# Kernel optimization log

Measured on AMD Instinct MI355X. Metric: run time of the kernel, lower is better.

The kernel has to match this reference:

```python
import jax, jax.numpy as jnp
import numpy as np

E, K = 8, 2
B, S, H = 8, 2048, 512
R0, R1, O = 256, 256, 512
T = B * S


def _make_routing(key):
    # Mixtral-style: top-k softmax weights [T, K] and one-hot mask [E, K, T]
    k1, k2 = jax.random.split(key)
    sel = jax.random.randint(k1, (T, K), 0, E)                      # selected expert per (token, slot)
    rw = jax.nn.softmax(jax.random.normal(k2, (T, K)), axis=-1)
    mask = jax.nn.one_hot(sel, E, dtype=jnp.bool_)                  # [T, K, E]
    mask = jnp.transpose(mask, (2, 1, 0))                           # [E, K, T]
    return mask, rw


def setup_inputs() -> dict:
    key = jax.random.key(0)
    ks = jax.random.split(key, 10)
    x = jax.random.normal(ks[0], (B, S, H), dtype=jnp.float32)
    m1, rw1 = _make_routing(ks[1])
    m2, rw2 = _make_routing(ks[2])
    m3, rw3 = _make_routing(ks[3])
    s = 0.02
    W1 = jax.random.normal(ks[4], (E, R0, H), dtype=jnp.float32) * s
    b1 = jnp.zeros((E, R0), dtype=jnp.float32)
    W2 = jax.random.normal(ks[5], (E, R1, R0), dtype=jnp.float32) * s
    b2 = jnp.zeros((E, R1), dtype=jnp.float32)
    W3 = jax.random.normal(ks[6], (E, O, R1), dtype=jnp.float32) * s
    b3 = jnp.zeros((E, O), dtype=jnp.float32)
    return {"x": x,
            "expert_mask1": m1, "expert_mask2": m2, "expert_mask3": m3,
            "routing_weights1": rw1, "routing_weights2": rw2, "routing_weights3": rw3,
            "W1": W1, "b1": b1, "W2": W2, "b2": b2, "W3": W3, "b3": b3}


def _moe_stage(h, mask, rw, W, b, act):
    # combine[e, t] = routing weight of token t for expert e (0 if not routed)
    cmb = jnp.einsum('ekt,tk->et', mask.astype(h.dtype), rw)
    acc0 = jnp.zeros((h.shape[0], W.shape[1]), dtype=h.dtype)

    def body(acc, ew):
        Wi, bi, ci = ew            # Wi: [out, in], bi: [out], ci: [T]
        out = h @ Wi.T + bi
        if act:
            out = jax.nn.relu(out)
        return acc + ci[:, None] * out, None

    acc, _ = jax.lax.scan(body, acc0, (W, b, cmb))
    return acc


def reference(x, expert_mask1, expert_mask2, expert_mask3,
              routing_weights1, routing_weights2, routing_weights3,
              W1, b1, W2, b2, W3, b3):
    bsz, seq, dim = x.shape
    h = x.reshape(-1, dim)                                          # [T, H]
    h = _moe_stage(h, expert_mask1, routing_weights1, W1, b1, act=False)   # [T, R0]
    h = _moe_stage(h, expert_mask2, routing_weights2, W2, b2, act=False)   # [T, R1]
    h = _moe_stage(h, expert_mask3, routing_weights3, W3, b3, act=True)    # relu on expert output, then combine
    out = jax.nn.relu(h.reshape(bsz, seq, -1))
    return out
```

## Files before the change

### kernel.cpp

```cpp
#include <hip/hip_runtime.h>

#define T_TOKENS 16384
#define CAP 12288
#define RB 96
#define CNT_STRIDE 16

typedef unsigned short u16;
typedef unsigned int u32;
typedef __attribute__((ext_vector_type(8))) short short8;
typedef __attribute__((ext_vector_type(4))) float float4v;

typedef __attribute__((address_space(1))) u32 gas_u32;
typedef __attribute__((address_space(3))) u32 las_u32;

__device__ __forceinline__ u16 f2b(float f) {
  unsigned u = __float_as_uint(f);
  u = (u + 0x7fffu + ((u >> 16) & 1u)) >> 16;
  return (u16)u;
}
__device__ __forceinline__ float b2f(u16 h) {
  return __uint_as_float(((unsigned)h) << 16);
}
__device__ __forceinline__ void gload16(const u16* g, u16* l) {
  __builtin_amdgcn_global_load_lds((gas_u32*)g, (las_u32*)l, 16, 0, 0);
}

__global__ void prep_kernel(const float* __restrict__ W1, const float* __restrict__ W2,
                            const float* __restrict__ W3,
                            const int* __restrict__ m1, const int* __restrict__ m2,
                            const int* __restrict__ m3, const float* __restrict__ rw1,
                            const float* __restrict__ rw2, const float* __restrict__ rw3,
                            u16* __restrict__ Wb1, u16* __restrict__ Wb2, u16* __restrict__ Wb3,
                            int* __restrict__ cnt, int* __restrict__ idxbuf,
                            float* __restrict__ wgtbuf) {
  __shared__ int lcnt[24];
  __shared__ int lbase[24];
  const int tid = threadIdx.x;

  if (blockIdx.x >= 64) {
    const int n1 = 8 * 256 * 512, n2 = 8 * 256 * 256;
    int base = (blockIdx.x - 64) * 2048 + tid * 8;
    const float* src;
    u16* dst;
    int off = base;
    if (base < n1) { src = W1; dst = Wb1; }
    else if (base < n1 + n2) { src = W2; dst = Wb2; off = base - n1; }
    else { src = W3; dst = Wb3; off = base - n1 - n2; }
    float4 a0 = *(const float4*)(src + off);
    float4 a1 = *(const float4*)(src + off + 4);
    short8 v;
    v[0] = (short)f2b(a0.x); v[1] = (short)f2b(a0.y);
    v[2] = (short)f2b(a0.z); v[3] = (short)f2b(a0.w);
    v[4] = (short)f2b(a1.x); v[5] = (short)f2b(a1.y);
    v[6] = (short)f2b(a1.z); v[7] = (short)f2b(a1.w);
    *(short8*)(dst + off) = v;
    return;
  }

  const int t = blockIdx.x * 256 + tid;
  if (tid < 24) lcnt[tid] = 0;
  __syncthreads();

  const int* masks[3] = {m1, m2, m3};
  const float* rws[3] = {rw1, rw2, rw3};
  int expert[3][2], lpos[3][2];
#pragma unroll
  for (int s = 0; s < 3; ++s)
#pragma unroll
    for (int k = 0; k < 2; ++k) {
      int e = 0;
#pragma unroll
      for (int j = 0; j < 8; ++j)
        if (masks[s][(j * 2 + k) * T_TOKENS + t] != 0) e = j;
      expert[s][k] = e;
      lpos[s][k] = atomicAdd(&lcnt[s * 8 + e], 1);
    }
  __syncthreads();
  if (tid < 24) lbase[tid] = atomicAdd(&cnt[tid * CNT_STRIDE], lcnt[tid]);
  __syncthreads();
#pragma unroll
  for (int s = 0; s < 3; ++s)
#pragma unroll
    for (int k = 0; k < 2; ++k) {
      int e = expert[s][k];
      int p = lbase[s * 8 + e] + lpos[s][k];
      if (p < CAP) {
        idxbuf[(s * 8 + e) * CAP + p] = t * 2 + k;
        wgtbuf[(s * 8 + e) * CAP + p] = rws[s][t * 2 + k];
      }
    }
}

template <int KDIM, int NDIM_TOTAL, int SRC, int RELU>
__global__ __launch_bounds__(256) void moe_gemm(
    const void* __restrict__ Asrc, const u16* __restrict__ Wb, const float* __restrict__ bias,
    const int* __restrict__ cnt, const int* __restrict__ idxbuf, const float* __restrict__ wgtbuf,
    u16* __restrict__ outTmp) {
  __shared__ __align__(16) u16 As[64 * 64];
  __shared__ __align__(16) u16 Bs[256 * 64];
  __shared__ int rowTok[64];
  __shared__ float rowW[64];

  const int e = blockIdx.y;
  const int n_e = cnt[e * CNT_STRIDE];
  const int row0 = blockIdx.x * 64;
  if (row0 >= n_e) return;
  const int nbase = blockIdx.z * 256;
  const int tid = threadIdx.x;

  if (tid < 64) {
    int g = row0 + tid;
    if (g < n_e) {
      rowTok[tid] = idxbuf[e * CAP + g];
      rowW[tid] = wgtbuf[e * CAP + g];
    } else {
      rowTok[tid] = 0;
      rowW[tid] = 0.f;
    }
  }
  __syncthreads();

  const int wave = tid >> 6, lane = tid & 63;
  const int lrow = lane & 15, lquad = lane >> 4;
  const int srow = lane >> 3;
  const int gswl = (lane & 7) ^ srow;

  const u16* Wbe = Wb + ((size_t)e * NDIM_TOTAL + nbase) * KDIM;
  const u16* bP = Wbe + (size_t)(wave * 64 + srow) * KDIM + gswl * 8;
  u16* bD = Bs + (wave * 8) * 512;

  const int arow = tid >> 3;
  const int gsrc = tid & 7;

  float4v acc[4][4];
#pragma unroll
  for (int i = 0; i < 4; ++i)
#pragma unroll
    for (int j = 0; j < 4; ++j) acc[i][j] = (float4v)0.f;

  for (int kb = 0; kb < KDIM; kb += 64) {
#pragma unroll
    for (int i = 0; i < 8; ++i)
      gload16(bP + (size_t)i * 8 * KDIM + kb, bD + i * 512);
#pragma unroll
    for (int it = 0; it < 2; ++it) {
      int r = arow + it * 32;
      int tok = rowTok[r];
      int slot = gsrc ^ (r & 7);
      short8 v;
      if (SRC == 0) {
        const float* xp = (const float*)Asrc + (size_t)(tok >> 1) * KDIM + kb + gsrc * 8;
        float4 a0 = *(const float4*)xp;
        float4 a1 = *(const float4*)(xp + 4);
        v[0] = (short)f2b(a0.x); v[1] = (short)f2b(a0.y);
        v[2] = (short)f2b(a0.z); v[3] = (short)f2b(a0.w);
        v[4] = (short)f2b(a1.x); v[5] = (short)f2b(a1.y);
        v[6] = (short)f2b(a1.z); v[7] = (short)f2b(a1.w);
      } else {
        const u16* p0 = (const u16*)Asrc + ((size_t)(tok >> 1) * 2) * KDIM + kb + gsrc * 8;
        short8 v0 = *(const short8*)p0;
        short8 v1 = *(const short8*)(p0 + KDIM);
#pragma unroll
        for (int j = 0; j < 8; ++j)
          v[j] = (short)f2b(b2f((u16)v0[j]) + b2f((u16)v1[j]));
      }
      *(short8*)&As[r * 64 + slot * 8] = v;
    }
    __syncthreads();
#pragma unroll
    for (int ks = 0; ks < 64; ks += 32) {
      const int gq = ((ks >> 3) + lquad) ^ (lrow & 7);
      short8 af[4], bfr[4];
#pragma unroll
      for (int mt = 0; mt < 4; ++mt)
        af[mt] = *(const short8*)&As[(mt * 16 + lrow) * 64 + gq * 8];
#pragma unroll
      for (int nt = 0; nt < 4; ++nt)
        bfr[nt] = *(const short8*)&Bs[(wave * 64 + nt * 16 + lrow) * 64 + gq * 8];
#pragma unroll
      for (int mt = 0; mt < 4; ++mt)
#pragma unroll
        for (int nt = 0; nt < 4; ++nt)
          acc[mt][nt] = __builtin_amdgcn_mfma_f32_16x16x32_bf16(af[mt], bfr[nt], acc[mt][nt], 0, 0, 0);
    }
    __syncthreads();
  }

  float bv[4];
#pragma unroll
  for (int nt = 0; nt < 4; ++nt)
    bv[nt] = bias[e * NDIM_TOTAL + nbase + wave * 64 + nt * 16 + lrow];
#pragma unroll
  for (int mt = 0; mt < 4; ++mt) {
#pragma unroll
    for (int i = 0; i < 4; ++i) {
      int m = mt * 16 + lquad * 4 + i;
      if (row0 + m < n_e) {
        float w = rowW[m];
        size_t drow = (size_t)rowTok[m] * NDIM_TOTAL + nbase;
#pragma unroll
        for (int nt = 0; nt < 4; ++nt) {
          float v = acc[mt][nt][i] + bv[nt];
          if (RELU) v = fmaxf(v, 0.f);
          v *= w;
          outTmp[drow + wave * 64 + nt * 16 + lrow] = f2b(v);
        }
      }
    }
  }
}

__global__ void finalize_kernel(const u16* __restrict__ tmp3, float* __restrict__ out) {
  int f = (blockIdx.x * 256 + threadIdx.x) * 8;
  int t = f >> 9;
  int o = f & 511;
  const u16* p = tmp3 + (size_t)t * 1024 + o;
  short8 v0 = *(const short8*)p;
  short8 v1 = *(const short8*)(p + 512);
  float4 r0, r1;
  r0.x = fmaxf(b2f((u16)v0[0]) + b2f((u16)v1[0]), 0.f);
  r0.y = fmaxf(b2f((u16)v0[1]) + b2f((u16)v1[1]), 0.f);
  r0.z = fmaxf(b2f((u16)v0[2]) + b2f((u16)v1[2]), 0.f);
  r0.w = fmaxf(b2f((u16)v0[3]) + b2f((u16)v1[3]), 0.f);
  r1.x = fmaxf(b2f((u16)v0[4]) + b2f((u16)v1[4]), 0.f);
  r1.y = fmaxf(b2f((u16)v0[5]) + b2f((u16)v1[5]), 0.f);
  r1.z = fmaxf(b2f((u16)v0[6]) + b2f((u16)v1[6]), 0.f);
  r1.w = fmaxf(b2f((u16)v0[7]) + b2f((u16)v1[7]), 0.f);
  *(float4*)(out + f) = r0;
  *(float4*)(out + f + 4) = r1;
}

extern "C" void kernel_launch(void* const* d_in, const int* in_sizes, int n_in,
                              void* d_out, int out_size, void* d_ws, size_t ws_size,
                              hipStream_t stream) {
  const float* x  = (const float*)d_in[0];
  const int* m1   = (const int*)d_in[1];
  const int* m2   = (const int*)d_in[2];
  const int* m3   = (const int*)d_in[3];
  const float* rw1 = (const float*)d_in[4];
  const float* rw2 = (const float*)d_in[5];
  const float* rw3 = (const float*)d_in[6];
  const float* W1 = (const float*)d_in[7];
  const float* b1 = (const float*)d_in[8];
  const float* W2 = (const float*)d_in[9];
  const float* b2 = (const float*)d_in[10];
  const float* W3 = (const float*)d_in[11];
  const float* b3 = (const float*)d_in[12];
  float* out = (float*)d_out;

  char* ws = (char*)d_ws;
  size_t off = 0;
  int* cnt = (int*)(ws + off); off += 24 * CNT_STRIDE * 4;
  u16* Wb1 = (u16*)(ws + off); off += (size_t)8 * 256 * 512 * 2;
  u16* Wb2 = (u16*)(ws + off); off += (size_t)8 * 256 * 256 * 2;
  u16* Wb3 = (u16*)(ws + off); off += (size_t)8 * 512 * 256 * 2;
  u16* tmp1 = (u16*)(ws + off); off += (size_t)T_TOKENS * 2 * 256 * 2;
  u16* tmp2 = (u16*)(ws + off); off += (size_t)T_TOKENS * 2 * 256 * 2;
  u16* tmp3 = (u16*)(ws + off); off += (size_t)T_TOKENS * 2 * 512 * 2;
  int* idxb = (int*)(ws + off); off += (size_t)3 * 8 * CAP * 4;
  float* wgtb = (float*)(ws + off); off += (size_t)3 * 8 * CAP * 4;

  hipMemsetAsync(cnt, 0, 24 * CNT_STRIDE * 4, stream);
  prep_kernel<<<1344, 256, 0, stream>>>(W1, W2, W3, m1, m2, m3, rw1, rw2, rw3,
                                        Wb1, Wb2, Wb3, cnt, idxb, wgtb);

  moe_gemm<512, 256, 0, 0><<<dim3(RB, 8, 1), 256, 0, stream>>>(
      x, Wb1, b1, cnt + 0, idxb + 0, wgtb + 0, tmp1);
  moe_gemm<256, 256, 1, 0><<<dim3(RB, 8, 1), 256, 0, stream>>>(
      tmp1, Wb2, b2, cnt + 8 * CNT_STRIDE, idxb + 8 * CAP, wgtb + 8 * CAP, tmp2);
  moe_gemm<256, 512, 1, 1><<<dim3(RB, 8, 2), 256, 0, stream>>>(
      tmp2, Wb3, b3, cnt + 16 * CNT_STRIDE, idxb + 16 * CAP, wgtb + 16 * CAP, tmp3);

  finalize_kernel<<<4096, 256, 0, stream>>>(tmp3, out);
}
```

Measured before the change: 184.2 us.

## Drop LDS staging in MoE GEMM and load MFMA fragments directly from global

The MoE GEMM no longer stages A and B tiles through shared memory. Each lane now loads its MFMA operand fragments straight from global memory using per-row token pointers, which removes the barriers and the LDS traffic. The input x is converted to bf16 once in the prep kernel, so stage 1 reads bf16 instead of converting fp32 inside the GEMM. The cost is that the four waves no longer share staged tiles, so there are redundant global/L2 reads of A and B, uncoalesced gathers, and extra bandwidth for the x conversion pass.

```diff
diff --git a/kernel.cpp b/kernel.cpp
--- a/kernel.cpp
+++ b/kernel.cpp
@@ -10,9 +10,6 @@
 typedef __attribute__((ext_vector_type(8))) short short8;
 typedef __attribute__((ext_vector_type(4))) float float4v;
 
-typedef __attribute__((address_space(1))) u32 gas_u32;
-typedef __attribute__((address_space(3))) u32 las_u32;
-
 __device__ __forceinline__ u16 f2b(float f) {
   unsigned u = __float_as_uint(f);
   u = (u + 0x7fffu + ((u >> 16) & 1u)) >> 16;
@@ -21,16 +18,14 @@
 __device__ __forceinline__ float b2f(u16 h) {
   return __uint_as_float(((unsigned)h) << 16);
 }
-__device__ __forceinline__ void gload16(const u16* g, u16* l) {
-  __builtin_amdgcn_global_load_lds((gas_u32*)g, (las_u32*)l, 16, 0, 0);
-}
 
 __global__ void prep_kernel(const float* __restrict__ W1, const float* __restrict__ W2,
-                            const float* __restrict__ W3,
+                            const float* __restrict__ W3, const float* __restrict__ x,
                             const int* __restrict__ m1, const int* __restrict__ m2,
                             const int* __restrict__ m3, const float* __restrict__ rw1,
                             const float* __restrict__ rw2, const float* __restrict__ rw3,
                             u16* __restrict__ Wb1, u16* __restrict__ Wb2, u16* __restrict__ Wb3,
+                            u16* __restrict__ xb,
                             int* __restrict__ cnt, int* __restrict__ idxbuf,
                             float* __restrict__ wgtbuf) {
   __shared__ int lcnt[24];
@@ -38,14 +33,15 @@
   const int tid = threadIdx.x;
 
   if (blockIdx.x >= 64) {
-    const int n1 = 8 * 256 * 512, n2 = 8 * 256 * 256;
+    const int n1 = 8 * 256 * 512, n2 = 8 * 256 * 256, n3 = 8 * 512 * 256;
     int base = (blockIdx.x - 64) * 2048 + tid * 8;
     const float* src;
     u16* dst;
     int off = base;
     if (base < n1) { src = W1; dst = Wb1; }
     else if (base < n1 + n2) { src = W2; dst = Wb2; off = base - n1; }
-    else { src = W3; dst = Wb3; off = base - n1 - n2; }
+    else if (base < n1 + n2 + n3) { src = W3; dst = Wb3; off = base - n1 - n2; }
+    else { src = x; dst = xb; off = base - n1 - n2 - n3; }
     float4 a0 = *(const float4*)(src + off);
     float4 a1 = *(const float4*)(src + off + 4);
     short8 v;
@@ -92,45 +88,36 @@
 }
 
 template <int KDIM, int NDIM_TOTAL, int SRC, int RELU>
-__global__ __launch_bounds__(256) void moe_gemm(
-    const void* __restrict__ Asrc, const u16* __restrict__ Wb, const float* __restrict__ bias,
+__global__ void moe_gemm(
+    const u16* __restrict__ Asrc, const u16* __restrict__ Wb, const float* __restrict__ bias,
     const int* __restrict__ cnt, const int* __restrict__ idxbuf, const float* __restrict__ wgtbuf,
     u16* __restrict__ outTmp) {
-  __shared__ __align__(16) u16 As[64 * 64];
-  __shared__ __align__(16) u16 Bs[256 * 64];
-  __shared__ int rowTok[64];
-  __shared__ float rowW[64];
-
   const int e = blockIdx.y;
   const int n_e = cnt[e * CNT_STRIDE];
   const int row0 = blockIdx.x * 64;
   if (row0 >= n_e) return;
   const int nbase = blockIdx.z * 256;
   const int tid = threadIdx.x;
-
-  if (tid < 64) {
-    int g = row0 + tid;
-    if (g < n_e) {
-      rowTok[tid] = idxbuf[e * CAP + g];
-      rowW[tid] = wgtbuf[e * CAP + g];
+  const int wc = tid >> 6, lane = tid & 63;
+  const int lrow = lane & 15, lquad = lane >> 4;
+
+  const u16* aB0[4];
+  const u16* aB1[4];
+#pragma unroll
+  for (int mt = 0; mt < 4; ++mt) {
+    int g = row0 + mt * 16 + lrow;
+    int tok = (g < n_e) ? idxbuf[e * CAP + g] : 0;
+    if constexpr (SRC == 0) {
+      aB0[mt] = Asrc + (size_t)(tok >> 1) * KDIM + lquad * 8;
     } else {
-      rowTok[tid] = 0;
-      rowW[tid] = 0.f;
-    }
-  }
-  __syncthreads();
-
-  const int wave = tid >> 6, lane = tid & 63;
-  const int lrow = lane & 15, lquad = lane >> 4;
-  const int srow = lane >> 3;
-  const int gswl = (lane & 7) ^ srow;
-
-  const u16* Wbe = Wb + ((size_t)e * NDIM_TOTAL + nbase) * KDIM;
-  const u16* bP = Wbe + (size_t)(wave * 64 + srow) * KDIM + gswl * 8;
-  u16* bD = Bs + (wave * 8) * 512;
-
-  const int arow = tid >> 3;
-  const int gsrc = tid & 7;
+      aB0[mt] = Asrc + ((size_t)(tok >> 1) * 2) * KDIM + lquad * 8;
+      aB1[mt] = aB0[mt] + KDIM;
+    }
+  }
+  const u16* bB[4];
+#pragma unroll
+  for (int nt = 0; nt < 4; ++nt)
+    bB[nt] = Wb + ((size_t)e * NDIM_TOTAL + nbase + wc * 64 + nt * 16 + lrow) * KDIM + lquad * 8;
 
   float4v acc[4][4];
 #pragma unroll
@@ -138,72 +125,50 @@
 #pragma unroll
     for (int j = 0; j < 4; ++j) acc[i][j] = (float4v)0.f;
 
-  for (int kb = 0; kb < KDIM; kb += 64) {
-#pragma unroll
-    for (int i = 0; i < 8; ++i)
-      gload16(bP + (size_t)i * 8 * KDIM + kb, bD + i * 512);
-#pragma unroll
-    for (int it = 0; it < 2; ++it) {
-      int r = arow + it * 32;
-      int tok = rowTok[r];
-      int slot = gsrc ^ (r & 7);
-      short8 v;
-      if (SRC == 0) {
-        const float* xp = (const float*)Asrc + (size_t)(tok >> 1) * KDIM + kb + gsrc * 8;
-        float4 a0 = *(const float4*)xp;
-        float4 a1 = *(const float4*)(xp + 4);
-        v[0] = (short)f2b(a0.x); v[1] = (short)f2b(a0.y);
-        v[2] = (short)f2b(a0.z); v[3] = (short)f2b(a0.w);
-        v[4] = (short)f2b(a1.x); v[5] = (short)f2b(a1.y);
-        v[6] = (short)f2b(a1.z); v[7] = (short)f2b(a1.w);
+#pragma unroll 2
+  for (int kb = 0; kb < KDIM; kb += 32) {
+    short8 af[4], bf[4];
+#pragma unroll
+    for (int mt = 0; mt < 4; ++mt) {
+      if constexpr (SRC == 0) {
+        af[mt] = *(const short8*)(aB0[mt] + kb);
       } else {
-        const u16* p0 = (const u16*)Asrc + ((size_t)(tok >> 1) * 2) * KDIM + kb + gsrc * 8;
-        short8 v0 = *(const short8*)p0;
-        short8 v1 = *(const short8*)(p0 + KDIM);
+        short8 u = *(const short8*)(aB0[mt] + kb);
+        short8 w = *(const short8*)(aB1[mt] + kb);
 #pragma unroll
         for (int j = 0; j < 8; ++j)
-          v[j] = (short)f2b(b2f((u16)v0[j]) + b2f((u16)v1[j]));
+          af[mt][j] = (short)f2b(b2f((u16)u[j]) + b2f((u16)w[j]));
       }
-      *(short8*)&As[r * 64 + slot * 8] = v;
-    }
-    __syncthreads();
-#pragma unroll
-    for (int ks = 0; ks < 64; ks += 32) {
-      const int gq = ((ks >> 3) + lquad) ^ (lrow & 7);
-      short8 af[4], bfr[4];
-#pragma unroll
-      for (int mt = 0; mt < 4; ++mt)
-        af[mt] = *(const short8*)&As[(mt * 16 + lrow) * 64 + gq * 8];
+    }
+#pragma unroll
+    for (int nt = 0; nt < 4; ++nt)
+      bf[nt] = *(const short8*)(bB[nt] + kb);
+#pragma unroll
+    for (int mt = 0; mt < 4; ++mt)
 #pragma unroll
       for (int nt = 0; nt < 4; ++nt)
-        bfr[nt] = *(const short8*)&Bs[(wave * 64 + nt * 16 + lrow) * 64 + gq * 8];
-#pragma unroll
-      for (int mt = 0; mt < 4; ++mt)
-#pragma unroll
-        for (int nt = 0; nt < 4; ++nt)
-          acc[mt][nt] = __builtin_amdgcn_mfma_f32_16x16x32_bf16(af[mt], bfr[nt], acc[mt][nt], 0, 0, 0);
-    }
-    __syncthreads();
+        acc[mt][nt] = __builtin_amdgcn_mfma_f32_16x16x32_bf16(af[mt], bf[nt], acc[mt][nt], 0, 0, 0);
   }
 
   float bv[4];
 #pragma unroll
   for (int nt = 0; nt < 4; ++nt)
-    bv[nt] = bias[e * NDIM_TOTAL + nbase + wave * 64 + nt * 16 + lrow];
+    bv[nt] = bias[e * NDIM_TOTAL + nbase + wc * 64 + nt * 16 + lrow];
 #pragma unroll
   for (int mt = 0; mt < 4; ++mt) {
 #pragma unroll
     for (int i = 0; i < 4; ++i) {
       int m = mt * 16 + lquad * 4 + i;
-      if (row0 + m < n_e) {
-        float w = rowW[m];
-        size_t drow = (size_t)rowTok[m] * NDIM_TOTAL + nbase;
+      int g = row0 + m;
+      if (g < n_e) {
+        float w = wgtbuf[e * CAP + g];
+        size_t drow = (size_t)idxbuf[e * CAP + g] * NDIM_TOTAL + nbase;
 #pragma unroll
         for (int nt = 0; nt < 4; ++nt) {
           float v = acc[mt][nt][i] + bv[nt];
           if (RELU) v = fmaxf(v, 0.f);
           v *= w;
-          outTmp[drow + wave * 64 + nt * 16 + lrow] = f2b(v);
+          outTmp[drow + wc * 64 + nt * 16 + lrow] = f2b(v);
         }
       }
     }
@@ -254,6 +219,7 @@
   u16* Wb1 = (u16*)(ws + off); off += (size_t)8 * 256 * 512 * 2;
   u16* Wb2 = (u16*)(ws + off); off += (size_t)8 * 256 * 256 * 2;
   u16* Wb3 = (u16*)(ws + off); off += (size_t)8 * 512 * 256 * 2;
+  u16* xb  = (u16*)(ws + off); off += (size_t)T_TOKENS * 512 * 2;
   u16* tmp1 = (u16*)(ws + off); off += (size_t)T_TOKENS * 2 * 256 * 2;
   u16* tmp2 = (u16*)(ws + off); off += (size_t)T_TOKENS * 2 * 256 * 2;
   u16* tmp3 = (u16*)(ws + off); off += (size_t)T_TOKENS * 2 * 512 * 2;
@@ -261,11 +227,11 @@
   float* wgtb = (float*)(ws + off); off += (size_t)3 * 8 * CAP * 4;
 
   hipMemsetAsync(cnt, 0, 24 * CNT_STRIDE * 4, stream);
-  prep_kernel<<<1344, 256, 0, stream>>>(W1, W2, W3, m1, m2, m3, rw1, rw2, rw3,
-                                        Wb1, Wb2, Wb3, cnt, idxb, wgtb);
+  prep_kernel<<<5440, 256, 0, stream>>>(W1, W2, W3, x, m1, m2, m3, rw1, rw2, rw3,
+                                        Wb1, Wb2, Wb3, xb, cnt, idxb, wgtb);
 
   moe_gemm<512, 256, 0, 0><<<dim3(RB, 8, 1), 256, 0, stream>>>(
-      x, Wb1, b1, cnt + 0, idxb + 0, wgtb + 0, tmp1);
+      xb, Wb1, b1, cnt + 0, idxb + 0, wgtb + 0, tmp1);
   moe_gemm<256, 256, 1, 0><<<dim3(RB, 8, 1), 256, 0, stream>>>(
       tmp1, Wb2, b2, cnt + 8 * CNT_STRIDE, idxb + 8 * CAP, wgtb + 8 * CAP, tmp2);
   moe_gemm<256, 512, 1, 1><<<dim3(RB, 8, 2), 256, 0, stream>>>(
```

Result: slower. 332.9 us (+80.8%).

## Split K dimension across blocks in first two MoE GEMM stages

Applied to the files above, without the earlier changes.

Stages 1 and 2 now split the reduction dimension into two halves, each run by its own block along grid z. Each half writes a separate partial output slot per token, so the intermediate buffers grow to four slots per token. The next stage sums all four slots while loading its A tile, and only the first half adds the bias. This doubles the block count for the underfilled early stages, at the cost of extra bf16 partial writes, more reads in the following stage, and an extra bf16 rounding of each partial.

```diff
diff --git a/kernel.cpp b/kernel.cpp
--- a/kernel.cpp
+++ b/kernel.cpp
@@ -91,7 +91,7 @@
     }
 }
 
-template <int KDIM, int NDIM_TOTAL, int SRC, int RELU>
+template <int KDIM, int NDIM_TOTAL, int SRC, int RELU, int KSPLIT, int SLOTS_IN>
 __global__ __launch_bounds__(256) void moe_gemm(
     const void* __restrict__ Asrc, const u16* __restrict__ Wb, const float* __restrict__ bias,
     const int* __restrict__ cnt, const int* __restrict__ idxbuf, const float* __restrict__ wgtbuf,
@@ -105,7 +105,10 @@
   const int n_e = cnt[e * CNT_STRIDE];
   const int row0 = blockIdx.x * 64;
   if (row0 >= n_e) return;
-  const int nbase = blockIdx.z * 256;
+  const int khalf = (KSPLIT > 1) ? blockIdx.z : 0;
+  const int nbase = (KSPLIT > 1) ? 0 : blockIdx.z * 256;
+  const int kbase = khalf * (KDIM / KSPLIT);
+  const int KLEN = KDIM / KSPLIT;
   const int tid = threadIdx.x;
 
   if (tid < 64) {
@@ -126,7 +129,7 @@
   const int gswl = (lane & 7) ^ srow;
 
   const u16* Wbe = Wb + ((size_t)e * NDIM_TOTAL + nbase) * KDIM;
-  const u16* bP = Wbe + (size_t)(wave * 64 + srow) * KDIM + gswl * 8;
+  const u16* bP = Wbe + (size_t)(wave * 64 + srow) * KDIM + kbase + gswl * 8;
   u16* bD = Bs + (wave * 8) * 512;
 
   const int arow = tid >> 3;
@@ -138,7 +141,7 @@
 #pragma unroll
     for (int j = 0; j < 4; ++j) acc[i][j] = (float4v)0.f;
 
-  for (int kb = 0; kb < KDIM; kb += 64) {
+  for (int kb = 0; kb < KLEN; kb += 64) {
 #pragma unroll
     for (int i = 0; i < 8; ++i)
       gload16(bP + (size_t)i * 8 * KDIM + kb, bD + i * 512);
@@ -149,7 +152,7 @@
       int slot = gsrc ^ (r & 7);
       short8 v;
       if (SRC == 0) {
-        const float* xp = (const float*)Asrc + (size_t)(tok >> 1) * KDIM + kb + gsrc * 8;
+        const float* xp = (const float*)Asrc + (size_t)(tok >> 1) * KDIM + kbase + kb + gsrc * 8;
         float4 a0 = *(const float4*)xp;
         float4 a1 = *(const float4*)(xp + 4);
         v[0] = (short)f2b(a0.x); v[1] = (short)f2b(a0.y);
@@ -157,12 +160,18 @@
         v[4] = (short)f2b(a1.x); v[5] = (short)f2b(a1.y);
         v[6] = (short)f2b(a1.z); v[7] = (short)f2b(a1.w);
       } else {
-        const u16* p0 = (const u16*)Asrc + ((size_t)(tok >> 1) * 2) * KDIM + kb + gsrc * 8;
-        short8 v0 = *(const short8*)p0;
-        short8 v1 = *(const short8*)(p0 + KDIM);
-#pragma unroll
-        for (int j = 0; j < 8; ++j)
-          v[j] = (short)f2b(b2f((u16)v0[j]) + b2f((u16)v1[j]));
+        const u16* p0 = (const u16*)Asrc + ((size_t)(tok >> 1) * SLOTS_IN) * KDIM + kbase + kb + gsrc * 8;
+        short8 sv[SLOTS_IN];
+#pragma unroll
+        for (int sl = 0; sl < SLOTS_IN; ++sl)
+          sv[sl] = *(const short8*)(p0 + (size_t)sl * KDIM);
+#pragma unroll
+        for (int j = 0; j < 8; ++j) {
+          float s = 0.f;
+#pragma unroll
+          for (int sl = 0; sl < SLOTS_IN; ++sl) s += b2f((u16)sv[sl][j]);
+          v[j] = (short)f2b(s);
+        }
       }
       *(short8*)&As[r * 64 + slot * 8] = v;
     }
@@ -190,6 +199,7 @@
 #pragma unroll
   for (int nt = 0; nt < 4; ++nt)
     bv[nt] = bias[e * NDIM_TOTAL + nbase + wave * 64 + nt * 16 + lrow];
+  const float bscale = (KSPLIT == 1 || khalf == 0) ? 1.f : 0.f;
 #pragma unroll
   for (int mt = 0; mt < 4; ++mt) {
 #pragma unroll
@@ -197,10 +207,11 @@
       int m = mt * 16 + lquad * 4 + i;
       if (row0 + m < n_e) {
         float w = rowW[m];
-        size_t drow = (size_t)rowTok[m] * NDIM_TOTAL + nbase;
+        size_t orow = (KSPLIT > 1) ? ((size_t)rowTok[m] * 2 + khalf) : (size_t)rowTok[m];
+        size_t drow = orow * NDIM_TOTAL + nbase;
 #pragma unroll
         for (int nt = 0; nt < 4; ++nt) {
-          float v = acc[mt][nt][i] + bv[nt];
+          float v = acc[mt][nt][i] + bv[nt] * bscale;
           if (RELU) v = fmaxf(v, 0.f);
           v *= w;
           outTmp[drow + wave * 64 + nt * 16 + lrow] = f2b(v);
@@ -254,8 +265,8 @@
   u16* Wb1 = (u16*)(ws + off); off += (size_t)8 * 256 * 512 * 2;
   u16* Wb2 = (u16*)(ws + off); off += (size_t)8 * 256 * 256 * 2;
   u16* Wb3 = (u16*)(ws + off); off += (size_t)8 * 512 * 256 * 2;
-  u16* tmp1 = (u16*)(ws + off); off += (size_t)T_TOKENS * 2 * 256 * 2;
-  u16* tmp2 = (u16*)(ws + off); off += (size_t)T_TOKENS * 2 * 256 * 2;
+  u16* tmp1 = (u16*)(ws + off); off += (size_t)T_TOKENS * 4 * 256 * 2;
+  u16* tmp2 = (u16*)(ws + off); off += (size_t)T_TOKENS * 4 * 256 * 2;
   u16* tmp3 = (u16*)(ws + off); off += (size_t)T_TOKENS * 2 * 512 * 2;
   int* idxb = (int*)(ws + off); off += (size_t)3 * 8 * CAP * 4;
   float* wgtb = (float*)(ws + off); off += (size_t)3 * 8 * CAP * 4;
@@ -264,11 +275,11 @@
   prep_kernel<<<1344, 256, 0, stream>>>(W1, W2, W3, m1, m2, m3, rw1, rw2, rw3,
                                         Wb1, Wb2, Wb3, cnt, idxb, wgtb);
 
-  moe_gemm<512, 256, 0, 0><<<dim3(RB, 8, 1), 256, 0, stream>>>(
+  moe_gemm<512, 256, 0, 0, 2, 1><<<dim3(RB, 8, 2), 256, 0, stream>>>(
       x, Wb1, b1, cnt + 0, idxb + 0, wgtb + 0, tmp1);
-  moe_gemm<256, 256, 1, 0><<<dim3(RB, 8, 1), 256, 0, stream>>>(
+  moe_gemm<256, 256, 1, 0, 2, 4><<<dim3(RB, 8, 2), 256, 0, stream>>>(
       tmp1, Wb2, b2, cnt + 8 * CNT_STRIDE, idxb + 8 * CAP, wgtb + 8 * CAP, tmp2);
-  moe_gemm<256, 512, 1, 1><<<dim3(RB, 8, 2), 256, 0, stream>>>(
+  moe_gemm<256, 512, 1, 1, 1, 4><<<dim3(RB, 8, 2), 256, 0, stream>>>(
       tmp2, Wb3, b3, cnt + 16 * CNT_STRIDE, idxb + 16 * CAP, wgtb + 16 * CAP, tmp3);
 
   finalize_kernel<<<4096, 256, 0, stream>>>(tmp3, out);
```

Result: slower. 207.9 us (+12.9%).
